# Performance work log

Hardware: AMD Instinct MI355X
Metric: run time of the kernel (lower is better)

## Reference

```python
import jax, jax.numpy as jnp
import numpy as np

DIM, HEADS, WS, SHIFT = 192, 6, 8, 4
EPS = 1e-5


def layer_norm(x, g, b):
    mu = jnp.mean(x, axis=-1, keepdims=True)
    var = jnp.mean(jnp.square(x - mu), axis=-1, keepdims=True)
    return (x - mu) * jax.lax.rsqrt(var + EPS) * g + b


def window_partition(x, ws):
    # x: [B, H, W, C] -> [B*nW, ws*ws, C]
    B, H, W, C = x.shape
    x = x.reshape(B, H // ws, ws, W // ws, ws, C)
    return x.transpose(0, 1, 3, 2, 4, 5).reshape(-1, ws * ws, C)


def window_merge(win, ws, B, H, W, C):
    x = win.reshape(B, H // ws, W // ws, ws, ws, C)
    return x.transpose(0, 1, 3, 2, 4, 5).reshape(B, H, W, C)


def make_shift_mask(H, W, ws, shift):
    # standard Swin attention mask for shifted windows (host-side constant)
    img = np.zeros((H, W), dtype=np.float32)
    cnt = 0
    slices = (slice(0, -ws), slice(-ws, -shift), slice(-shift, None))
    for hs in slices:
        for wsl in slices:
            img[hs, wsl] = cnt
            cnt += 1
    m = img.reshape(H // ws, ws, W // ws, ws).transpose(0, 2, 1, 3).reshape(-1, ws * ws)  # [nW, N]
    diff = m[:, None, :] - m[:, :, None]
    return jnp.asarray(np.where(diff != 0, -100.0, 0.0).astype(np.float32))  # [nW, N, N]


def swin_attention(x, qkv_w, qkv_b, proj_w, proj_b, shift):
    B, H, W, C = x.shape
    h, d = HEADS, C // HEADS
    scale = 1.0 / jnp.sqrt(jnp.asarray(d, x.dtype))
    if shift > 0:
        x = jnp.roll(x, shift=(-shift, -shift), axis=(1, 2))
    win = window_partition(x, WS)                       # [Bn, N, C]
    Bn, N, _ = win.shape
    qkv = win @ qkv_w + qkv_b                           # [Bn, N, 3C]
    qkv = qkv.reshape(Bn, N, 3, h, d).transpose(2, 0, 3, 1, 4)
    q, k, v = qkv[0], qkv[1], qkv[2]                    # [Bn, h, N, d]
    attn = jnp.einsum('bhnd,bhmd->bhnm', q, k) * scale  # [Bn, h, N, N]
    if shift > 0:
        mask = make_shift_mask(H, W, WS, shift)         # [nW, N, N]
        nW = mask.shape[0]
        attn = attn.reshape(Bn // nW, nW, h, N, N) + mask[None, :, None]
        attn = attn.reshape(Bn, h, N, N)
    attn = jax.nn.softmax(attn, axis=-1)
    out = jnp.einsum('bhnm,bhmd->bhnd', attn, v)        # [Bn, h, N, d]
    out = out.transpose(0, 2, 1, 3).reshape(Bn, N, C)
    out = out @ proj_w + proj_b
    out = window_merge(out, WS, B, H, W, C)
    if shift > 0:
        out = jnp.roll(out, shift=(shift, shift), axis=(1, 2))
    return out


def setup_inputs() -> dict:
    key = jax.random.key(0)
    ks = jax.random.split(key, 6)
    B, H, W, C = 8, 128, 128, DIM
    s = 0.02
    return {
        'x': jax.random.normal(ks[0], (B, H, W, C), jnp.float32),
        'ln1_g': jnp.ones((C,), jnp.float32),
        'ln1_b': jnp.zeros((C,), jnp.float32),
        'qkv1_w': jax.random.normal(ks[1], (C, 3 * C), jnp.float32) * s,
        'qkv1_b': jnp.zeros((3 * C,), jnp.float32),
        'proj1_w': jax.random.normal(ks[2], (C, C), jnp.float32) * s,
        'proj1_b': jnp.zeros((C,), jnp.float32),
        'ln2_g': jnp.ones((C,), jnp.float32),
        'ln2_b': jnp.zeros((C,), jnp.float32),
        'qkv2_w': jax.random.normal(ks[3], (C, 3 * C), jnp.float32) * s,
        'qkv2_b': jnp.zeros((3 * C,), jnp.float32),
        'proj2_w': jax.random.normal(ks[4], (C, C), jnp.float32) * s,
        'proj2_b': jnp.zeros((C,), jnp.float32),
    }


def reference(x, ln1_g, ln1_b, qkv1_w, qkv1_b, proj1_w, proj1_b,
              ln2_g, ln2_b, qkv2_w, qkv2_b, proj2_w, proj2_b):
    # W-MSA branch (mlp1 is an empty Sequential -> identity)
    y = layer_norm(x, ln1_g, ln1_b)
    x = x + swin_attention(y, qkv1_w, qkv1_b, proj1_w, proj1_b, shift=0)
    # SW-MSA branch (mlp2 is identity)
    y = layer_norm(x, ln2_g, ln2_b)
    x = x + swin_attention(y, qkv2_w, qkv2_b, proj2_w, proj2_b, shift=SHIFT)
    return x
```

## Files before the change

### kernel.cpp

```cpp
#include <hip/hip_runtime.h>

typedef unsigned int   u32;
typedef unsigned short u16;
typedef __bf16 bf16x8 __attribute__((ext_vector_type(8)));
typedef float  f32x4  __attribute__((ext_vector_type(4)));

__device__ __forceinline__ u16 f2bf(float f) {
    u32 u = __builtin_bit_cast(u32, f);
    u += 0x7FFFu + ((u >> 16) & 1u);
    return (u16)(u >> 16);
}
__device__ __forceinline__ u32 cvtpk(float a, float b) {
    u32 r;
    asm("v_cvt_pk_bf16_f32 %0, %1, %2" : "=v"(r) : "v"(a), "v"(b));
    return r;
}
__device__ __forceinline__ bf16x8 ldfrag(const u16* p) {
    return __builtin_bit_cast(bf16x8, *reinterpret_cast<const uint4*>(p));
}

__device__ __forceinline__ u32 swz(u32 i) { return i ^ ((i >> 3) & 7u); }

template<int SHIFT>
__global__ __launch_bounds__(768) void swin_branch(
    const float* __restrict__ xin, float* __restrict__ xout,
    const float* __restrict__ ln_g, const float* __restrict__ ln_b,
    const u16*   __restrict__ wqkv_t,
    const float* __restrict__ qkv_b,
    const u16*   __restrict__ wproj_t,
    const float* __restrict__ proj_b)
{
    __shared__ __align__(16) u16 smem[49152];
    __shared__ float red1[2][6][64];
    __shared__ float red2[2][6][64];
    constexpr u32 QOFF = 12288;
    constexpr float QSC = 0.17677669529663689f * 1.4426950408889634f;

    const int tid  = threadIdx.x;
    const int win  = (tid >= 384) ? 1 : 0;
    const int lt   = tid - win*384;
    const int wid  = lt >> 6;
    const int lane = lt & 63;
    const int lr   = lane & 15;
    const int lg   = lane >> 4;
    const u32 lsw  = swz((u32)lane);
    const u32 SB   = (u32)win * 24576u;

    const int Wid = blockIdx.x*2 + win;
    const int b   = Wid >> 8;
    const int wy  = (Wid >> 4) & 15;
    const int wx  = Wid & 15;

    {
        const int ty = lane >> 3, tx = lane & 7;
        const int shy = (wy*8 + ty + SHIFT) & 127;
        const int shx = (wx*8 + tx + SHIFT) & 127;
        const float* xp = xin + ((size_t)((b*128 + shy)*128 + shx))*192 + wid*32;
        float xv[32];
        float s1 = 0.f, s2 = 0.f;
        #pragma unroll
        for (int j = 0; j < 8; ++j) {
            float4 v = reinterpret_cast<const float4*>(xp)[j];
            xv[j*4+0]=v.x; xv[j*4+1]=v.y; xv[j*4+2]=v.z; xv[j*4+3]=v.w;
            s1 += v.x+v.y+v.z+v.w;
            s2 += v.x*v.x + v.y*v.y + v.z*v.z + v.w*v.w;
        }
        red1[win][wid][lane] = s1; red2[win][wid][lane] = s2;
        __syncthreads();
        float a1 = 0.f, a2 = 0.f;
        #pragma unroll
        for (int w = 0; w < 6; ++w) { a1 += red1[win][w][lane]; a2 += red2[win][w][lane]; }
        const float mu = a1 * (1.f/192.f);
        const float rs = rsqrtf(a2 * (1.f/192.f) - mu*mu + 1e-5f);
        const float* gp = ln_g + wid*32;
        const float* bp = ln_b + wid*32;
        const u32 yblk = SB + (u32)((lg*6 + wid)*512);
        #pragma unroll
        for (int cc8 = 0; cc8 < 4; ++cc8) {
            u32 pk[4];
            #pragma unroll
            for (int q = 0; q < 4; ++q) {
                int j = cc8*8 + q*2;
                float y0 = (xv[j]   - mu)*rs*gp[j]   + bp[j];
                float y1 = (xv[j+1] - mu)*rs*gp[j+1] + bp[j+1];
                pk[q] = cvtpk(y0, y1);
            }
            *reinterpret_cast<uint4*>(&smem[yblk + swz((u32)(lr + 16*cc8))*8]) =
                make_uint4(pk[0],pk[1],pk[2],pk[3]);
        }
    }
    __syncthreads();

    uint2 kpk[4][2];
    uint2 vpk[4][2];
    {
        {
            f32x4 acc[4][4];
            #pragma unroll
            for (int mi=0; mi<4; ++mi)
                #pragma unroll
                for (int t=0; t<4; ++t) acc[mi][t] = f32x4{0.f,0.f,0.f,0.f};
            #pragma unroll
            for (int ks=0; ks<6; ++ks) {
                bf16x8 af[4];
                #pragma unroll
                for (int mi=0; mi<4; ++mi)
                    af[mi] = ldfrag(&smem[SB + (u32)((mi*6+ks)*512) + lsw*8]);
                bf16x8 bw[4];
                #pragma unroll
                for (int t=0; t<4; ++t)
                    bw[t] = ldfrag(&wqkv_t[((t>>1)*192 + wid*32 + (t&1)*16 + lr)*192 + 32*ks + 8*lg]);
                #pragma unroll
                for (int mi=0; mi<4; ++mi)
                    #pragma unroll
                    for (int t=0; t<4; ++t)
                        acc[mi][t] = __builtin_amdgcn_mfma_f32_16x16x32_bf16(bw[t], af[mi], acc[mi][t], 0,0,0);
            }
            #pragma unroll
            for (int t=0; t<2; ++t) {
                const float4 b4 = *reinterpret_cast<const float4*>(&qkv_b[wid*32 + t*16 + 4*lg]);
                const u32 chunk = (u32)lr + 16u*(u32)(2*t + (lg>>1));
                #pragma unroll
                for (int mi=0; mi<4; ++mi) {
                    float v0 = (acc[mi][t][0] + b4.x) * QSC;
                    float v1 = (acc[mi][t][1] + b4.y) * QSC;
                    float v2 = (acc[mi][t][2] + b4.z) * QSC;
                    float v3 = (acc[mi][t][3] + b4.w) * QSC;
                    *reinterpret_cast<uint2*>(
                        &smem[SB + QOFF + (u32)(wid*2048) + mi*512 + swz(chunk)*8 + 4*(lg&1)]) =
                        make_uint2(cvtpk(v0,v1), cvtpk(v2,v3));
                }
            }
            #pragma unroll
            for (int t2=0; t2<2; ++t2) {
                const float4 b4 = *reinterpret_cast<const float4*>(&qkv_b[192 + wid*32 + t2*16 + 4*lg]);
                #pragma unroll
                for (int mi=0; mi<4; ++mi)
                    kpk[mi][t2] = make_uint2(
                        cvtpk(acc[mi][2+t2][0] + b4.x, acc[mi][2+t2][1] + b4.y),
                        cvtpk(acc[mi][2+t2][2] + b4.z, acc[mi][2+t2][3] + b4.w));
            }
        }
        {
            f32x4 acc[4][2];
            #pragma unroll
            for (int mi=0; mi<4; ++mi)
                #pragma unroll
                for (int t=0; t<2; ++t) acc[mi][t] = f32x4{0.f,0.f,0.f,0.f};
            #pragma unroll
            for (int ks=0; ks<6; ++ks) {
                bf16x8 af[4];
                #pragma unroll
                for (int mi=0; mi<4; ++mi)
                    af[mi] = ldfrag(&smem[SB + (u32)((mi*6+ks)*512) + lsw*8]);
                bf16x8 bw[2];
                #pragma unroll
                for (int t=0; t<2; ++t)
                    bw[t] = ldfrag(&wqkv_t[(384 + wid*32 + t*16 + lr)*192 + 32*ks + 8*lg]);
                #pragma unroll
                for (int mi=0; mi<4; ++mi)
                    #pragma unroll
                    for (int t=0; t<2; ++t)
                        acc[mi][t] = __builtin_amdgcn_mfma_f32_16x16x32_bf16(af[mi], bw[t], acc[mi][t], 0,0,0);
            }
            #pragma unroll
            for (int tv=0; tv<2; ++tv) {
                const float bias = qkv_b[384 + wid*32 + tv*16 + lr];
                #pragma unroll
                for (int mi=0; mi<4; ++mi)
                    vpk[mi][tv] = make_uint2(
                        cvtpk(acc[mi][tv][0] + bias, acc[mi][tv][1] + bias),
                        cvtpk(acc[mi][tv][2] + bias, acc[mi][tv][3] + bias));
            }
        }
    }
    __syncthreads();

    float rsum[4];
    f32x4 o_[2][4];
    {
        const u32 W  = SB + (u32)(wid*512);
        const u32 QB = SB + QOFF + (u32)(wid*2048);
        #define BLK(s) ((u32)(s)*3072u + W)

        #pragma unroll
        for (int t2=0; t2<2; ++t2) {
            const u32 chunk = (u32)lr + 16u*(u32)(2*t2 + (lg>>1));
            #pragma unroll
            for (int mi=0; mi<4; ++mi)
                *reinterpret_cast<uint2*>(
                    &smem[BLK(mi) + swz(chunk)*8 + 4*(lg&1)]) = kpk[mi][t2];
        }
        bf16x8 ak[4], bq[4];
        #pragma unroll
        for (int mi=0; mi<4; ++mi) ak[mi] = ldfrag(&smem[BLK(mi) + lsw*8]);
        #pragma unroll
        for (int nq=0; nq<4; ++nq) bq[nq] = ldfrag(&smem[QB + nq*512 + lsw*8]);
        __builtin_amdgcn_sched_barrier(0);

        int qcl[4];
        if constexpr (SHIFT > 0) {
            #pragma unroll
            for (int nq=0; nq<4; ++nq) {
                const int qt = 16*nq + lr;
                const int hu = wy*8 + (qt>>3);
                const int wu = wx*8 + (qt&7);
                qcl[nq] = ((hu >= 124) ? 2 : (hu >= 120 ? 1 : 0))*3
                        + ((wu >= 124) ? 2 : (wu >= 120 ? 1 : 0));
            }
        }

        uint2 p16[4][4];
        #pragma unroll
        for (int mi=0; mi<4; ++mi) {
            f32x4 sr[4];
            #pragma unroll
            for (int nq=0; nq<4; ++nq)
                sr[nq] = __builtin_amdgcn_mfma_f32_16x16x32_bf16(ak[mi], bq[nq],
                             f32x4{0.f,0.f,0.f,0.f}, 0,0,0);
            #pragma unroll
            for (int rg=0; rg<4; ++rg) {
                int kcl = 0;
                if constexpr (SHIFT > 0) {
                    const int kt = 16*mi + 4*lg + rg;
                    const int hu = wy*8 + (kt>>3);
                    const int wu = wx*8 + (kt&7);
                    kcl = ((hu >= 124) ? 2 : (hu >= 120 ? 1 : 0))*3
                        + ((wu >= 124) ? 2 : (wu >= 120 ? 1 : 0));
                }
                #pragma unroll
                for (int nq=0; nq<4; ++nq) {
                    float e = exp2f(sr[nq][rg]);
                    if constexpr (SHIFT > 0)
                        e = (kcl == qcl[nq]) ? e : 0.f;
                    sr[nq][rg] = e;
                }
            }
            #pragma unroll
            for (int nq=0; nq<4; ++nq)
                p16[mi][nq] = make_uint2(cvtpk(sr[nq][0], sr[nq][1]),
                                         cvtpk(sr[nq][2], sr[nq][3]));
        }

        #pragma unroll
        for (int mi=0; mi<4; ++mi) {
            const u32 chunk = (u32)lr + 16u*(u32)(2*(mi&1) + (lg>>1));
            #pragma unroll
            for (int nq=0; nq<4; ++nq) {
                const u32 base = (mi >> 1) ? BLK(nq) : (QB + nq*512);
                *reinterpret_cast<uint2*>(&smem[base + swz(chunk)*8 + 4*(lg&1)]) = p16[mi][nq];
            }
        }
        bf16x8 bp[4][2];
        #pragma unroll
        for (int nq=0; nq<4; ++nq) {
            bp[nq][0] = ldfrag(&smem[QB + nq*512 + lsw*8]);
            bp[nq][1] = ldfrag(&smem[BLK(nq) + lsw*8]);
        }
        __builtin_amdgcn_sched_barrier(0);

        bf16x8 aones;
        {
            const u32 one2 = 0x3F803F80u;
            aones = __builtin_bit_cast(bf16x8, make_uint4(one2, one2, one2, one2));
        }
        #pragma unroll
        for (int nq=0; nq<4; ++nq) {
            f32x4 racc = __builtin_amdgcn_mfma_f32_16x16x32_bf16(aones, bp[nq][0],
                             f32x4{0.f,0.f,0.f,0.f}, 0,0,0);
            racc = __builtin_amdgcn_mfma_f32_16x16x32_bf16(aones, bp[nq][1], racc, 0,0,0);
            rsum[nq] = __builtin_amdgcn_rcpf(racc[0]);
        }

        #pragma unroll
        for (int mi=0; mi<4; ++mi) {
            const u32 chunk = (u32)lr + 16u*(u32)(2*(mi&1) + (lg>>1));
            #pragma unroll
            for (int tv=0; tv<2; ++tv)
                *reinterpret_cast<uint2*>(
                    &smem[QB + (u32)((2*tv + (mi>>1))*512) + swz(chunk)*8 + 4*(lg&1)]) = vpk[mi][tv];
        }
        bf16x8 av[2][2];
        #pragma unroll
        for (int dv=0; dv<2; ++dv)
            #pragma unroll
            for (int ks=0; ks<2; ++ks)
                av[dv][ks] = ldfrag(&smem[QB + (u32)((2*dv + ks)*512) + lsw*8]);
        __builtin_amdgcn_sched_barrier(0);

        #pragma unroll
        for (int dv=0; dv<2; ++dv)
            #pragma unroll
            for (int nq=0; nq<4; ++nq) {
                o_[dv][nq] = __builtin_amdgcn_mfma_f32_16x16x32_bf16(av[dv][0], bp[nq][0],
                                 f32x4{0.f,0.f,0.f,0.f}, 0,0,0);
                o_[dv][nq] = __builtin_amdgcn_mfma_f32_16x16x32_bf16(av[dv][1], bp[nq][1],
                                 o_[dv][nq], 0,0,0);
            }
        __builtin_amdgcn_sched_barrier(0);

        #pragma unroll
        for (int dv=0; dv<2; ++dv) {
            const u32 chunk = (u32)lr + 16u*(u32)(2*dv + (lg>>1));
            #pragma unroll
            for (int nq=0; nq<4; ++nq) {
                const float r = rsum[nq];
                *reinterpret_cast<uint2*>(&smem[BLK(nq) + swz(chunk)*8 + 4*(lg&1)]) =
                    make_uint2(cvtpk(o_[dv][nq][0]*r, o_[dv][nq][1]*r),
                               cvtpk(o_[dv][nq][2]*r, o_[dv][nq][3]*r));
            }
        }
        #undef BLK
    }
    __syncthreads();

    {
        f32x4 a2[4][2];
        #pragma unroll
        for (int mi=0; mi<4; ++mi)
            #pragma unroll
            for (int ni=0; ni<2; ++ni) a2[mi][ni] = f32x4{0.f,0.f,0.f,0.f};
        #pragma unroll
        for (int ks=0; ks<6; ++ks) {
            bf16x8 af[4], bw[2];
            #pragma unroll
            for (int mi=0; mi<4; ++mi)
                af[mi] = ldfrag(&smem[SB + (u32)((mi*6+ks)*512) + lsw*8]);
            #pragma unroll
            for (int ni=0; ni<2; ++ni)
                bw[ni] = ldfrag(&wproj_t[(wid*32 + 16*ni + lr)*192 + 32*ks + 8*lg]);
            #pragma unroll
            for (int mi=0; mi<4; ++mi)
                #pragma unroll
                for (int ni=0; ni<2; ++ni)
                    a2[mi][ni] = __builtin_amdgcn_mfma_f32_16x16x32_bf16(af[mi], bw[ni], a2[mi][ni], 0,0,0);
        }
        #pragma unroll
        for (int ni=0; ni<2; ++ni) {
            const int c  = wid*32 + 16*ni + lr;
            const float pb = proj_b[c];
            #pragma unroll
            for (int mi=0; mi<4; ++mi)
                #pragma unroll
                for (int rg=0; rg<4; ++rg) {
                    const int row = 16*mi + 4*lg + rg;
                    const int ty = row >> 3, tx = row & 7;
                    const int shy = (wy*8 + ty + SHIFT) & 127;
                    const int shx = (wx*8 + tx + SHIFT) & 127;
                    const size_t idx = ((size_t)((b*128 + shy)*128 + shx))*192 + c;
                    xout[idx] = xin[idx] + a2[mi][ni][rg] + pb;
                }
        }
    }
}

__global__ void prep_weights(const float* __restrict__ qkv1, const float* __restrict__ proj1,
                             const float* __restrict__ qkv2, const float* __restrict__ proj2,
                             u16* __restrict__ ws)
{
    const int i = blockIdx.x*blockDim.x + threadIdx.x;
    if (i < 110592) {
        const int n = i / 192, k = i - n*192;
        ws[i]          = f2bf(qkv1[k*576 + n]);
        ws[147456 + i] = f2bf(qkv2[k*576 + n]);
    }
    if (i < 36864) {
        const int n = i / 192, k = i - n*192;
        ws[110592 + i] = f2bf(proj1[k*192 + n]);
        ws[258048 + i] = f2bf(proj2[k*192 + n]);
    }
}

extern "C" void kernel_launch(void* const* d_in, const int* in_sizes, int n_in,
                              void* d_out, int out_size, void* d_ws, size_t ws_size,
                              hipStream_t stream)
{
    const float* x       = (const float*)d_in[0];
    const float* ln1_g   = (const float*)d_in[1];
    const float* ln1_b   = (const float*)d_in[2];
    const float* qkv1_w  = (const float*)d_in[3];
    const float* qkv1_b  = (const float*)d_in[4];
    const float* proj1_w = (const float*)d_in[5];
    const float* proj1_b = (const float*)d_in[6];
    const float* ln2_g   = (const float*)d_in[7];
    const float* ln2_b   = (const float*)d_in[8];
    const float* qkv2_w  = (const float*)d_in[9];
    const float* qkv2_b  = (const float*)d_in[10];
    const float* proj2_w = (const float*)d_in[11];
    const float* proj2_b = (const float*)d_in[12];
    float* out = (float*)d_out;
    u16*   wsp = (u16*)d_ws;

    prep_weights<<<dim3(432), dim3(256), 0, stream>>>(qkv1_w, proj1_w, qkv2_w, proj2_w, wsp);
    swin_branch<0><<<dim3(1024), dim3(768), 0, stream>>>(x,   out, ln1_g, ln1_b,
                                                         wsp,        qkv1_b, wsp+110592, proj1_b);
    swin_branch<4><<<dim3(1024), dim3(768), 0, stream>>>(out, out, ln2_g, ln2_b,
                                                         wsp+147456, qkv2_b, wsp+258048, proj2_b);
}
```

Baseline: 262.8 us.

## Make attention kernel persistent with phase-staggered window processing across half-blocks

The kernel becomes persistent: 256 blocks each process four window pairs in a 22-step phase loop instead of launching 1024 blocks. The two 384-thread halves of a block are offset by two phases, so one half's global loads and LayerNorm overlap the other half's MFMA work, with one block-wide barrier per phase. This is meant to hide load latency and cut launch and tail overhead, at the cost of fewer blocks than CUs and extra barriers in which idle halves still wait.

```diff
diff --git a/kernel.cpp b/kernel.cpp
--- a/kernel.cpp
+++ b/kernel.cpp
@@ -45,312 +45,316 @@
     const int lg   = lane >> 4;
     const u32 lsw  = swz((u32)lane);
     const u32 SB   = (u32)win * 24576u;
-
-    const int Wid = blockIdx.x*2 + win;
-    const int b   = Wid >> 8;
-    const int wy  = (Wid >> 4) & 15;
-    const int wx  = Wid & 15;
-
-    {
-        const int ty = lane >> 3, tx = lane & 7;
-        const int shy = (wy*8 + ty + SHIFT) & 127;
-        const int shx = (wx*8 + tx + SHIFT) & 127;
-        const float* xp = xin + ((size_t)((b*128 + shy)*128 + shx))*192 + wid*32;
-        float xv[32];
-        float s1 = 0.f, s2 = 0.f;
-        #pragma unroll
-        for (int j = 0; j < 8; ++j) {
-            float4 v = reinterpret_cast<const float4*>(xp)[j];
-            xv[j*4+0]=v.x; xv[j*4+1]=v.y; xv[j*4+2]=v.z; xv[j*4+3]=v.w;
-            s1 += v.x+v.y+v.z+v.w;
-            s2 += v.x*v.x + v.y*v.y + v.z*v.z + v.w*v.w;
-        }
-        red1[win][wid][lane] = s1; red2[win][wid][lane] = s2;
-        __syncthreads();
-        float a1 = 0.f, a2 = 0.f;
-        #pragma unroll
-        for (int w = 0; w < 6; ++w) { a1 += red1[win][w][lane]; a2 += red2[win][w][lane]; }
-        const float mu = a1 * (1.f/192.f);
-        const float rs = rsqrtf(a2 * (1.f/192.f) - mu*mu + 1e-5f);
-        const float* gp = ln_g + wid*32;
-        const float* bp = ln_b + wid*32;
-        const u32 yblk = SB + (u32)((lg*6 + wid)*512);
-        #pragma unroll
-        for (int cc8 = 0; cc8 < 4; ++cc8) {
-            u32 pk[4];
-            #pragma unroll
-            for (int q = 0; q < 4; ++q) {
-                int j = cc8*8 + q*2;
-                float y0 = (xv[j]   - mu)*rs*gp[j]   + bp[j];
-                float y1 = (xv[j+1] - mu)*rs*gp[j+1] + bp[j+1];
-                pk[q] = cvtpk(y0, y1);
-            }
-            *reinterpret_cast<uint4*>(&smem[yblk + swz((u32)(lr + 16*cc8))*8]) =
-                make_uint4(pk[0],pk[1],pk[2],pk[3]);
-        }
-    }
-    __syncthreads();
-
+    const int ty   = lane >> 3, tx = lane & 7;
+
+    float xv[32];
     uint2 kpk[4][2];
     uint2 vpk[4][2];
-    {
-        {
-            f32x4 acc[4][4];
-            #pragma unroll
-            for (int mi=0; mi<4; ++mi)
-                #pragma unroll
-                for (int t=0; t<4; ++t) acc[mi][t] = f32x4{0.f,0.f,0.f,0.f};
-            #pragma unroll
-            for (int ks=0; ks<6; ++ks) {
-                bf16x8 af[4];
+    int b = 0, wy = 0, wx = 0;
+
+    #pragma unroll 1
+    for (int t = 0; t < 22; ++t) {
+        const int ph = t - 2*win;
+        if (ph >= 0 && ph < 20) {
+            const int widx = ph / 5;
+            const int p    = ph - widx*5;
+
+            if (p == 0) {
+                const int Wid = (widx*256 + (int)blockIdx.x)*2 + win;
+                b = Wid >> 8; wy = (Wid >> 4) & 15; wx = Wid & 15;
+                const int shy = (wy*8 + ty + SHIFT) & 127;
+                const int shx = (wx*8 + tx + SHIFT) & 127;
+                const float* xp = xin + ((size_t)((b*128 + shy)*128 + shx))*192 + wid*32;
+                float s1 = 0.f, s2 = 0.f;
+                #pragma unroll
+                for (int j = 0; j < 8; ++j) {
+                    float4 v = reinterpret_cast<const float4*>(xp)[j];
+                    xv[j*4+0]=v.x; xv[j*4+1]=v.y; xv[j*4+2]=v.z; xv[j*4+3]=v.w;
+                    s1 += v.x+v.y+v.z+v.w;
+                    s2 += v.x*v.x + v.y*v.y + v.z*v.z + v.w*v.w;
+                }
+                red1[win][wid][lane] = s1; red2[win][wid][lane] = s2;
+
+            } else if (p == 1) {
+                float a1 = 0.f, a2 = 0.f;
+                #pragma unroll
+                for (int w = 0; w < 6; ++w) { a1 += red1[win][w][lane]; a2 += red2[win][w][lane]; }
+                const float mu = a1 * (1.f/192.f);
+                const float rs = rsqrtf(a2 * (1.f/192.f) - mu*mu + 1e-5f);
+                const float* gp = ln_g + wid*32;
+                const float* bp = ln_b + wid*32;
+                const u32 yblk = SB + (u32)((lg*6 + wid)*512);
+                #pragma unroll
+                for (int cc8 = 0; cc8 < 4; ++cc8) {
+                    u32 pk[4];
+                    #pragma unroll
+                    for (int q = 0; q < 4; ++q) {
+                        int j = cc8*8 + q*2;
+                        float y0 = (xv[j]   - mu)*rs*gp[j]   + bp[j];
+                        float y1 = (xv[j+1] - mu)*rs*gp[j+1] + bp[j+1];
+                        pk[q] = cvtpk(y0, y1);
+                    }
+                    *reinterpret_cast<uint4*>(&smem[yblk + swz((u32)(lr + 16*cc8))*8]) =
+                        make_uint4(pk[0],pk[1],pk[2],pk[3]);
+                }
+
+            } else if (p == 2) {
+                {
+                    f32x4 acc[4][4];
+                    #pragma unroll
+                    for (int mi=0; mi<4; ++mi)
+                        #pragma unroll
+                        for (int q=0; q<4; ++q) acc[mi][q] = f32x4{0.f,0.f,0.f,0.f};
+                    #pragma unroll
+                    for (int ks=0; ks<6; ++ks) {
+                        bf16x8 af[4];
+                        #pragma unroll
+                        for (int mi=0; mi<4; ++mi)
+                            af[mi] = ldfrag(&smem[SB + (u32)((mi*6+ks)*512) + lsw*8]);
+                        bf16x8 bw[4];
+                        #pragma unroll
+                        for (int q=0; q<4; ++q)
+                            bw[q] = ldfrag(&wqkv_t[((q>>1)*192 + wid*32 + (q&1)*16 + lr)*192 + 32*ks + 8*lg]);
+                        #pragma unroll
+                        for (int mi=0; mi<4; ++mi)
+                            #pragma unroll
+                            for (int q=0; q<4; ++q)
+                                acc[mi][q] = __builtin_amdgcn_mfma_f32_16x16x32_bf16(bw[q], af[mi], acc[mi][q], 0,0,0);
+                    }
+                    #pragma unroll
+                    for (int q=0; q<2; ++q) {
+                        const float4 b4 = *reinterpret_cast<const float4*>(&qkv_b[wid*32 + q*16 + 4*lg]);
+                        const u32 chunk = (u32)lr + 16u*(u32)(2*q + (lg>>1));
+                        #pragma unroll
+                        for (int mi=0; mi<4; ++mi) {
+                            float v0 = (acc[mi][q][0] + b4.x) * QSC;
+                            float v1 = (acc[mi][q][1] + b4.y) * QSC;
+                            float v2 = (acc[mi][q][2] + b4.z) * QSC;
+                            float v3 = (acc[mi][q][3] + b4.w) * QSC;
+                            *reinterpret_cast<uint2*>(
+                                &smem[SB + QOFF + (u32)(wid*2048) + mi*512 + swz(chunk)*8 + 4*(lg&1)]) =
+                                make_uint2(cvtpk(v0,v1), cvtpk(v2,v3));
+                        }
+                    }
+                    #pragma unroll
+                    for (int t2=0; t2<2; ++t2) {
+                        const float4 b4 = *reinterpret_cast<const float4*>(&qkv_b[192 + wid*32 + t2*16 + 4*lg]);
+                        #pragma unroll
+                        for (int mi=0; mi<4; ++mi)
+                            kpk[mi][t2] = make_uint2(
+                                cvtpk(acc[mi][2+t2][0] + b4.x, acc[mi][2+t2][1] + b4.y),
+                                cvtpk(acc[mi][2+t2][2] + b4.z, acc[mi][2+t2][3] + b4.w));
+                    }
+                }
+                {
+                    f32x4 acc[4][2];
+                    #pragma unroll
+                    for (int mi=0; mi<4; ++mi)
+                        #pragma unroll
+                        for (int q=0; q<2; ++q) acc[mi][q] = f32x4{0.f,0.f,0.f,0.f};
+                    #pragma unroll
+                    for (int ks=0; ks<6; ++ks) {
+                        bf16x8 af[4];
+                        #pragma unroll
+                        for (int mi=0; mi<4; ++mi)
+                            af[mi] = ldfrag(&smem[SB + (u32)((mi*6+ks)*512) + lsw*8]);
+                        bf16x8 bw[2];
+                        #pragma unroll
+                        for (int q=0; q<2; ++q)
+                            bw[q] = ldfrag(&wqkv_t[(384 + wid*32 + q*16 + lr)*192 + 32*ks + 8*lg]);
+                        #pragma unroll
+                        for (int mi=0; mi<4; ++mi)
+                            #pragma unroll
+                            for (int q=0; q<2; ++q)
+                                acc[mi][q] = __builtin_amdgcn_mfma_f32_16x16x32_bf16(af[mi], bw[q], acc[mi][q], 0,0,0);
+                    }
+                    #pragma unroll
+                    for (int tv=0; tv<2; ++tv) {
+                        const float bias = qkv_b[384 + wid*32 + tv*16 + lr];
+                        #pragma unroll
+                        for (int mi=0; mi<4; ++mi)
+                            vpk[mi][tv] = make_uint2(
+                                cvtpk(acc[mi][tv][0] + bias, acc[mi][tv][1] + bias),
+                                cvtpk(acc[mi][tv][2] + bias, acc[mi][tv][3] + bias));
+                    }
+                }
+
+            } else if (p == 3) {
+                float rsum[4];
+                f32x4 o_[2][4];
+                const u32 W  = SB + (u32)(wid*512);
+                const u32 QB = SB + QOFF + (u32)(wid*2048);
+                #define BLK(s) ((u32)(s)*3072u + W)
+
+                #pragma unroll
+                for (int t2=0; t2<2; ++t2) {
+                    const u32 chunk = (u32)lr + 16u*(u32)(2*t2 + (lg>>1));
+                    #pragma unroll
+                    for (int mi=0; mi<4; ++mi)
+                        *reinterpret_cast<uint2*>(
+                            &smem[BLK(mi) + swz(chunk)*8 + 4*(lg&1)]) = kpk[mi][t2];
+                }
+                bf16x8 ak[4], bq[4];
+                #pragma unroll
+                for (int mi=0; mi<4; ++mi) ak[mi] = ldfrag(&smem[BLK(mi) + lsw*8]);
+                #pragma unroll
+                for (int nq=0; nq<4; ++nq) bq[nq] = ldfrag(&smem[QB + nq*512 + lsw*8]);
+                __builtin_amdgcn_sched_barrier(0);
+
+                int qcl[4];
+                if constexpr (SHIFT > 0) {
+                    #pragma unroll
+                    for (int nq=0; nq<4; ++nq) {
+                        const int qt = 16*nq + lr;
+                        const int hu = wy*8 + (qt>>3);
+                        const int wu = wx*8 + (qt&7);
+                        qcl[nq] = ((hu >= 124) ? 2 : (hu >= 120 ? 1 : 0))*3
+                                + ((wu >= 124) ? 2 : (wu >= 120 ? 1 : 0));
+                    }
+                }
+
+                uint2 p16[4][4];
+                #pragma unroll
+                for (int mi=0; mi<4; ++mi) {
+                    f32x4 sr[4];
+                    #pragma unroll
+                    for (int nq=0; nq<4; ++nq)
+                        sr[nq] = __builtin_amdgcn_mfma_f32_16x16x32_bf16(ak[mi], bq[nq],
+                                     f32x4{0.f,0.f,0.f,0.f}, 0,0,0);
+                    #pragma unroll
+                    for (int rg=0; rg<4; ++rg) {
+                        int kcl = 0;
+                        if constexpr (SHIFT > 0) {
+                            const int kt = 16*mi + 4*lg + rg;
+                            const int hu = wy*8 + (kt>>3);
+                            const int wu = wx*8 + (kt&7);
+                            kcl = ((hu >= 124) ? 2 : (hu >= 120 ? 1 : 0))*3
+                                + ((wu >= 124) ? 2 : (wu >= 120 ? 1 : 0));
+                        }
+                        #pragma unroll
+                        for (int nq=0; nq<4; ++nq) {
+                            float e = exp2f(sr[nq][rg]);
+                            if constexpr (SHIFT > 0)
+                                e = (kcl == qcl[nq]) ? e : 0.f;
+                            sr[nq][rg] = e;
+                        }
+                    }
+                    #pragma unroll
+                    for (int nq=0; nq<4; ++nq)
+                        p16[mi][nq] = make_uint2(cvtpk(sr[nq][0], sr[nq][1]),
+                                                 cvtpk(sr[nq][2], sr[nq][3]));
+                }
+
+                #pragma unroll
+                for (int mi=0; mi<4; ++mi) {
+                    const u32 chunk = (u32)lr + 16u*(u32)(2*(mi&1) + (lg>>1));
+                    #pragma unroll
+                    for (int nq=0; nq<4; ++nq) {
+                        const u32 base = (mi >> 1) ? BLK(nq) : (QB + nq*512);
+                        *reinterpret_cast<uint2*>(&smem[base + swz(chunk)*8 + 4*(lg&1)]) = p16[mi][nq];
+                    }
+                }
+                bf16x8 bp[4][2];
+                #pragma unroll
+                for (int nq=0; nq<4; ++nq) {
+                    bp[nq][0] = ldfrag(&smem[QB + nq*512 + lsw*8]);
+                    bp[nq][1] = ldfrag(&smem[BLK(nq) + lsw*8]);
+                }
+                __builtin_amdgcn_sched_barrier(0);
+
+                bf16x8 aones;
+                {
+                    const u32 one2 = 0x3F803F80u;
+                    aones = __builtin_bit_cast(bf16x8, make_uint4(one2, one2, one2, one2));
+                }
+                #pragma unroll
+                for (int nq=0; nq<4; ++nq) {
+                    f32x4 racc = __builtin_amdgcn_mfma_f32_16x16x32_bf16(aones, bp[nq][0],
+                                     f32x4{0.f,0.f,0.f,0.f}, 0,0,0);
+                    racc = __builtin_amdgcn_mfma_f32_16x16x32_bf16(aones, bp[nq][1], racc, 0,0,0);
+                    rsum[nq] = __builtin_amdgcn_rcpf(racc[0]);
+                }
+
+                #pragma unroll
+                for (int mi=0; mi<4; ++mi) {
+                    const u32 chunk = (u32)lr + 16u*(u32)(2*(mi&1) + (lg>>1));
+                    #pragma unroll
+                    for (int tv=0; tv<2; ++tv)
+                        *reinterpret_cast<uint2*>(
+                            &smem[QB + (u32)((2*tv + (mi>>1))*512) + swz(chunk)*8 + 4*(lg&1)]) = vpk[mi][tv];
+                }
+                bf16x8 av[2][2];
+                #pragma unroll
+                for (int dv=0; dv<2; ++dv)
+                    #pragma unroll
+                    for (int ks=0; ks<2; ++ks)
+                        av[dv][ks] = ldfrag(&smem[QB + (u32)((2*dv + ks)*512) + lsw*8]);
+                __builtin_amdgcn_sched_barrier(0);
+
+                #pragma unroll
+                for (int dv=0; dv<2; ++dv)
+                    #pragma unroll
+                    for (int nq=0; nq<4; ++nq) {
+                        o_[dv][nq] = __builtin_amdgcn_mfma_f32_16x16x32_bf16(av[dv][0], bp[nq][0],
+                                         f32x4{0.f,0.f,0.f,0.f}, 0,0,0);
+                        o_[dv][nq] = __builtin_amdgcn_mfma_f32_16x16x32_bf16(av[dv][1], bp[nq][1],
+                                         o_[dv][nq], 0,0,0);
+                    }
+                __builtin_amdgcn_sched_barrier(0);
+
+                #pragma unroll
+                for (int dv=0; dv<2; ++dv) {
+                    const u32 chunk = (u32)lr + 16u*(u32)(2*dv + (lg>>1));
+                    #pragma unroll
+                    for (int nq=0; nq<4; ++nq) {
+                        const float r = rsum[nq];
+                        *reinterpret_cast<uint2*>(&smem[BLK(nq) + swz(chunk)*8 + 4*(lg&1)]) =
+                            make_uint2(cvtpk(o_[dv][nq][0]*r, o_[dv][nq][1]*r),
+                                       cvtpk(o_[dv][nq][2]*r, o_[dv][nq][3]*r));
+                    }
+                }
+                #undef BLK
+
+            } else {
+                f32x4 a2[4][2];
                 #pragma unroll
                 for (int mi=0; mi<4; ++mi)
-                    af[mi] = ldfrag(&smem[SB + (u32)((mi*6+ks)*512) + lsw*8]);
-                bf16x8 bw[4];
-                #pragma unroll
-                for (int t=0; t<4; ++t)
-                    bw[t] = ldfrag(&wqkv_t[((t>>1)*192 + wid*32 + (t&1)*16 + lr)*192 + 32*ks + 8*lg]);
-                #pragma unroll
-                for (int mi=0; mi<4; ++mi)
-                    #pragma unroll
-                    for (int t=0; t<4; ++t)
-                        acc[mi][t] = __builtin_amdgcn_mfma_f32_16x16x32_bf16(bw[t], af[mi], acc[mi][t], 0,0,0);
-            }
-            #pragma unroll
-            for (int t=0; t<2; ++t) {
-                const float4 b4 = *reinterpret_cast<const float4*>(&qkv_b[wid*32 + t*16 + 4*lg]);
-                const u32 chunk = (u32)lr + 16u*(u32)(2*t + (lg>>1));
-                #pragma unroll
-                for (int mi=0; mi<4; ++mi) {
-                    float v0 = (acc[mi][t][0] + b4.x) * QSC;
-                    float v1 = (acc[mi][t][1] + b4.y) * QSC;
-                    float v2 = (acc[mi][t][2] + b4.z) * QSC;
-                    float v3 = (acc[mi][t][3] + b4.w) * QSC;
-                    *reinterpret_cast<uint2*>(
-                        &smem[SB + QOFF + (u32)(wid*2048) + mi*512 + swz(chunk)*8 + 4*(lg&1)]) =
-                        make_uint2(cvtpk(v0,v1), cvtpk(v2,v3));
-                }
-            }
-            #pragma unroll
-            for (int t2=0; t2<2; ++t2) {
-                const float4 b4 = *reinterpret_cast<const float4*>(&qkv_b[192 + wid*32 + t2*16 + 4*lg]);
-                #pragma unroll
-                for (int mi=0; mi<4; ++mi)
-                    kpk[mi][t2] = make_uint2(
-                        cvtpk(acc[mi][2+t2][0] + b4.x, acc[mi][2+t2][1] + b4.y),
-                        cvtpk(acc[mi][2+t2][2] + b4.z, acc[mi][2+t2][3] + b4.w));
+                    #pragma unroll
+                    for (int ni=0; ni<2; ++ni) a2[mi][ni] = f32x4{0.f,0.f,0.f,0.f};
+                #pragma unroll
+                for (int ks=0; ks<6; ++ks) {
+                    bf16x8 af[4], bw[2];
+                    #pragma unroll
+                    for (int mi=0; mi<4; ++mi)
+                        af[mi] = ldfrag(&smem[SB + (u32)((mi*6+ks)*512) + lsw*8]);
+                    #pragma unroll
+                    for (int ni=0; ni<2; ++ni)
+                        bw[ni] = ldfrag(&wproj_t[(wid*32 + 16*ni + lr)*192 + 32*ks + 8*lg]);
+                    #pragma unroll
+                    for (int mi=0; mi<4; ++mi)
+                        #pragma unroll
+                        for (int ni=0; ni<2; ++ni)
+                            a2[mi][ni] = __builtin_amdgcn_mfma_f32_16x16x32_bf16(af[mi], bw[ni], a2[mi][ni], 0,0,0);
+                }
+                #pragma unroll
+                for (int ni=0; ni<2; ++ni) {
+                    const int c  = wid*32 + 16*ni + lr;
+                    const float pb = proj_b[c];
+                    #pragma unroll
+                    for (int mi=0; mi<4; ++mi)
+                        #pragma unroll
+                        for (int rg=0; rg<4; ++rg) {
+                            const int row = 16*mi + 4*lg + rg;
+                            const int ty2 = row >> 3, tx2 = row & 7;
+                            const int shy = (wy*8 + ty2 + SHIFT) & 127;
+                            const int shx = (wx*8 + tx2 + SHIFT) & 127;
+                            const size_t idx = ((size_t)((b*128 + shy)*128 + shx))*192 + c;
+                            xout[idx] = xin[idx] + a2[mi][ni][rg] + pb;
+                        }
+                }
             }
         }
-        {
-            f32x4 acc[4][2];
-            #pragma unroll
-            for (int mi=0; mi<4; ++mi)
-                #pragma unroll
-                for (int t=0; t<2; ++t) acc[mi][t] = f32x4{0.f,0.f,0.f,0.f};
-            #pragma unroll
-            for (int ks=0; ks<6; ++ks) {
-                bf16x8 af[4];
-                #pragma unroll
-                for (int mi=0; mi<4; ++mi)
-                    af[mi] = ldfrag(&smem[SB + (u32)((mi*6+ks)*512) + lsw*8]);
-                bf16x8 bw[2];
-                #pragma unroll
-                for (int t=0; t<2; ++t)
-                    bw[t] = ldfrag(&wqkv_t[(384 + wid*32 + t*16 + lr)*192 + 32*ks + 8*lg]);
-                #pragma unroll
-                for (int mi=0; mi<4; ++mi)
-                    #pragma unroll
-                    for (int t=0; t<2; ++t)
-                        acc[mi][t] = __builtin_amdgcn_mfma_f32_16x16x32_bf16(af[mi], bw[t], acc[mi][t], 0,0,0);
-            }
-            #pragma unroll
-            for (int tv=0; tv<2; ++tv) {
-                const float bias = qkv_b[384 + wid*32 + tv*16 + lr];
-                #pragma unroll
-                for (int mi=0; mi<4; ++mi)
-                    vpk[mi][tv] = make_uint2(
-                        cvtpk(acc[mi][tv][0] + bias, acc[mi][tv][1] + bias),
-                        cvtpk(acc[mi][tv][2] + bias, acc[mi][tv][3] + bias));
-            }
-        }
-    }
-    __syncthreads();
-
-    float rsum[4];
-    f32x4 o_[2][4];
-    {
-        const u32 W  = SB + (u32)(wid*512);
-        const u32 QB = SB + QOFF + (u32)(wid*2048);
-        #define BLK(s) ((u32)(s)*3072u + W)
-
-        #pragma unroll
-        for (int t2=0; t2<2; ++t2) {
-            const u32 chunk = (u32)lr + 16u*(u32)(2*t2 + (lg>>1));
-            #pragma unroll
-            for (int mi=0; mi<4; ++mi)
-                *reinterpret_cast<uint2*>(
-                    &smem[BLK(mi) + swz(chunk)*8 + 4*(lg&1)]) = kpk[mi][t2];
-        }
-        bf16x8 ak[4], bq[4];
-        #pragma unroll
-        for (int mi=0; mi<4; ++mi) ak[mi] = ldfrag(&smem[BLK(mi) + lsw*8]);
-        #pragma unroll
-        for (int nq=0; nq<4; ++nq) bq[nq] = ldfrag(&smem[QB + nq*512 + lsw*8]);
-        __builtin_amdgcn_sched_barrier(0);
-
-        int qcl[4];
-        if constexpr (SHIFT > 0) {
-            #pragma unroll
-            for (int nq=0; nq<4; ++nq) {
-                const int qt = 16*nq + lr;
-                const int hu = wy*8 + (qt>>3);
-                const int wu = wx*8 + (qt&7);
-                qcl[nq] = ((hu >= 124) ? 2 : (hu >= 120 ? 1 : 0))*3
-                        + ((wu >= 124) ? 2 : (wu >= 120 ? 1 : 0));
-            }
-        }
-
-        uint2 p16[4][4];
-        #pragma unroll
-        for (int mi=0; mi<4; ++mi) {
-            f32x4 sr[4];
-            #pragma unroll
-            for (int nq=0; nq<4; ++nq)
-                sr[nq] = __builtin_amdgcn_mfma_f32_16x16x32_bf16(ak[mi], bq[nq],
-                             f32x4{0.f,0.f,0.f,0.f}, 0,0,0);
-            #pragma unroll
-            for (int rg=0; rg<4; ++rg) {
-                int kcl = 0;
-                if constexpr (SHIFT > 0) {
-                    const int kt = 16*mi + 4*lg + rg;
-                    const int hu = wy*8 + (kt>>3);
-                    const int wu = wx*8 + (kt&7);
-                    kcl = ((hu >= 124) ? 2 : (hu >= 120 ? 1 : 0))*3
-                        + ((wu >= 124) ? 2 : (wu >= 120 ? 1 : 0));
-                }
-                #pragma unroll
-                for (int nq=0; nq<4; ++nq) {
-                    float e = exp2f(sr[nq][rg]);
-                    if constexpr (SHIFT > 0)
-                        e = (kcl == qcl[nq]) ? e : 0.f;
-                    sr[nq][rg] = e;
-                }
-            }
-            #pragma unroll
-            for (int nq=0; nq<4; ++nq)
-                p16[mi][nq] = make_uint2(cvtpk(sr[nq][0], sr[nq][1]),
-                                         cvtpk(sr[nq][2], sr[nq][3]));
-        }
-
-        #pragma unroll
-        for (int mi=0; mi<4; ++mi) {
-            const u32 chunk = (u32)lr + 16u*(u32)(2*(mi&1) + (lg>>1));
-            #pragma unroll
-            for (int nq=0; nq<4; ++nq) {
-                const u32 base = (mi >> 1) ? BLK(nq) : (QB + nq*512);
-                *reinterpret_cast<uint2*>(&smem[base + swz(chunk)*8 + 4*(lg&1)]) = p16[mi][nq];
-            }
-        }
-        bf16x8 bp[4][2];
-        #pragma unroll
-        for (int nq=0; nq<4; ++nq) {
-            bp[nq][0] = ldfrag(&smem[QB + nq*512 + lsw*8]);
-            bp[nq][1] = ldfrag(&smem[BLK(nq) + lsw*8]);
-        }
-        __builtin_amdgcn_sched_barrier(0);
-
-        bf16x8 aones;
-        {
-            const u32 one2 = 0x3F803F80u;
-            aones = __builtin_bit_cast(bf16x8, make_uint4(one2, one2, one2, one2));
-        }
-        #pragma unroll
-        for (int nq=0; nq<4; ++nq) {
-            f32x4 racc = __builtin_amdgcn_mfma_f32_16x16x32_bf16(aones, bp[nq][0],
-                             f32x4{0.f,0.f,0.f,0.f}, 0,0,0);
-            racc = __builtin_amdgcn_mfma_f32_16x16x32_bf16(aones, bp[nq][1], racc, 0,0,0);
-            rsum[nq] = __builtin_amdgcn_rcpf(racc[0]);
-        }
-
-        #pragma unroll
-        for (int mi=0; mi<4; ++mi) {
-            const u32 chunk = (u32)lr + 16u*(u32)(2*(mi&1) + (lg>>1));
-            #pragma unroll
-            for (int tv=0; tv<2; ++tv)
-                *reinterpret_cast<uint2*>(
-                    &smem[QB + (u32)((2*tv + (mi>>1))*512) + swz(chunk)*8 + 4*(lg&1)]) = vpk[mi][tv];
-        }
-        bf16x8 av[2][2];
-        #pragma unroll
-        for (int dv=0; dv<2; ++dv)
-            #pragma unroll
-            for (int ks=0; ks<2; ++ks)
-                av[dv][ks] = ldfrag(&smem[QB + (u32)((2*dv + ks)*512) + lsw*8]);
-        __builtin_amdgcn_sched_barrier(0);
-
-        #pragma unroll
-        for (int dv=0; dv<2; ++dv)
-            #pragma unroll
-            for (int nq=0; nq<4; ++nq) {
-                o_[dv][nq] = __builtin_amdgcn_mfma_f32_16x16x32_bf16(av[dv][0], bp[nq][0],
-                                 f32x4{0.f,0.f,0.f,0.f}, 0,0,0);
-                o_[dv][nq] = __builtin_amdgcn_mfma_f32_16x16x32_bf16(av[dv][1], bp[nq][1],
-                                 o_[dv][nq], 0,0,0);
-            }
-        __builtin_amdgcn_sched_barrier(0);
-
-        #pragma unroll
-        for (int dv=0; dv<2; ++dv) {
-            const u32 chunk = (u32)lr + 16u*(u32)(2*dv + (lg>>1));
-            #pragma unroll
-            for (int nq=0; nq<4; ++nq) {
-                const float r = rsum[nq];
-                *reinterpret_cast<uint2*>(&smem[BLK(nq) + swz(chunk)*8 + 4*(lg&1)]) =
-                    make_uint2(cvtpk(o_[dv][nq][0]*r, o_[dv][nq][1]*r),
-                               cvtpk(o_[dv][nq][2]*r, o_[dv][nq][3]*r));
-            }
-        }
-        #undef BLK
-    }
-    __syncthreads();
-
-    {
-        f32x4 a2[4][2];
-        #pragma unroll
-        for (int mi=0; mi<4; ++mi)
-            #pragma unroll
-            for (int ni=0; ni<2; ++ni) a2[mi][ni] = f32x4{0.f,0.f,0.f,0.f};
-        #pragma unroll
-        for (int ks=0; ks<6; ++ks) {
-            bf16x8 af[4], bw[2];
-            #pragma unroll
-            for (int mi=0; mi<4; ++mi)
-                af[mi] = ldfrag(&smem[SB + (u32)((mi*6+ks)*512) + lsw*8]);
-            #pragma unroll
-            for (int ni=0; ni<2; ++ni)
-                bw[ni] = ldfrag(&wproj_t[(wid*32 + 16*ni + lr)*192 + 32*ks + 8*lg]);
-            #pragma unroll
-            for (int mi=0; mi<4; ++mi)
-                #pragma unroll
-                for (int ni=0; ni<2; ++ni)
-                    a2[mi][ni] = __builtin_amdgcn_mfma_f32_16x16x32_bf16(af[mi], bw[ni], a2[mi][ni], 0,0,0);
-        }
-        #pragma unroll
-        for (int ni=0; ni<2; ++ni) {
-            const int c  = wid*32 + 16*ni + lr;
-            const float pb = proj_b[c];
-            #pragma unroll
-            for (int mi=0; mi<4; ++mi)
-                #pragma unroll
-                for (int rg=0; rg<4; ++rg) {
-                    const int row = 16*mi + 4*lg + rg;
-                    const int ty = row >> 3, tx = row & 7;
-                    const int shy = (wy*8 + ty + SHIFT) & 127;
-                    const int shx = (wx*8 + tx + SHIFT) & 127;
-                    const size_t idx = ((size_t)((b*128 + shy)*128 + shx))*192 + c;
-                    xout[idx] = xin[idx] + a2[mi][ni][rg] + pb;
-                }
-        }
+        __syncthreads();
     }
 }
 
@@ -392,8 +396,8 @@
     u16*   wsp = (u16*)d_ws;
 
     prep_weights<<<dim3(432), dim3(256), 0, stream>>>(qkv1_w, proj1_w, qkv2_w, proj2_w, wsp);
-    swin_branch<0><<<dim3(1024), dim3(768), 0, stream>>>(x,   out, ln1_g, ln1_b,
-                                                         wsp,        qkv1_b, wsp+110592, proj1_b);
-    swin_branch<4><<<dim3(1024), dim3(768), 0, stream>>>(out, out, ln2_g, ln2_b,
-                                                         wsp+147456, qkv2_b, wsp+258048, proj2_b);
-}
+    swin_branch<0><<<dim3(256), dim3(768), 0, stream>>>(x,   out, ln1_g, ln1_b,
+                                                        wsp,        qkv1_b, wsp+110592, proj1_b);
+    swin_branch<4><<<dim3(256), dim3(768), 0, stream>>>(out, out, ln2_g, ln2_b,
+                                                        wsp+147456, qkv2_b, wsp+258048, proj2_b);
+}
```

After: 488.9 us. 1.86x slower.
